# Optimization experiments

Hardware: AMD Instinct MI355X
Metric: run time of the kernel (lower is better)

Reference implementation:

```python
import jax, jax.numpy as jnp
import numpy as np

B, D = 32768, 256
M, K, V = 1024, 128, 128  # memory_units, key_size, memory_size


def setup_inputs() -> dict:
    key = jax.random.key(0)
    ks = jax.random.split(key, 13)
    g = lambda k, shape, fan: jax.random.normal(k, shape, jnp.float32) * (2.0 / sum(fan)) ** 0.5
    return {
        "x": jax.random.normal(ks[0], (B, D), jnp.float32),
        "Wk": g(ks[1], (D, K), (D, K)), "bk": jnp.zeros((K,), jnp.float32),
        "Wv": g(ks[2], (D, V), (D, V)), "bv": jnp.zeros((V,), jnp.float32),
        "Wq": g(ks[3], (D, K), (D, K)), "bq": jnp.zeros((K,), jnp.float32),
        "Wwr": g(ks[4], (M, M), (M, M)), "bwr": jnp.zeros((M,), jnp.float32),
        "Wrd": g(ks[5], (M, M), (M, M)), "brd": jnp.zeros((M,), jnp.float32),
        "key_memory": g(ks[6], (M, K), (M, K)),
        "value_memory": g(ks[7], (M, V), (M, V)),
    }


def reference(x, Wk, bk, Wv, bv, Wq, bq, Wwr, bwr, Wrd, brd, key_memory, value_memory):
    elu = jax.nn.elu
    key_vec = elu(x @ Wk + bk)      # [B, K]
    val_vec = elu(x @ Wv + bv)      # [B, V]
    qry_vec = elu(x @ Wq + bq)      # [B, K]

    # write attention: Dense(M, softmax) applied to [B, M] scores
    wscores = key_vec @ key_memory.T            # [B, M]
    write_w = jax.nn.softmax(wscores @ Wwr + bwr, axis=-1)  # [B, M]

    inv_b = jnp.float32(1.0 / B)
    # mean over batch of outer products == einsum / B (avoids [B, M, K] intermediate)
    key_mem_new = key_memory + jnp.einsum("bm,bk->mk", write_w, key_vec) * inv_b
    val_mem_new = value_memory + jnp.einsum("bm,bv->mv", write_w, val_vec) * inv_b

    # read uses the UPDATED memories (matches assign_add ordering in call)
    rscores = qry_vec @ key_mem_new.T            # [B, M]
    read_w = jax.nn.softmax(rscores @ Wrd + brd, axis=-1)
    read_vec = read_w @ val_mem_new              # [B, V]
    return read_vec
```

## Files before the change

### kernel.cpp

```cpp
#include <hip/hip_runtime.h>
#include <stdint.h>


typedef short bf16x8 __attribute__((ext_vector_type(8)));
typedef short s16x4  __attribute__((ext_vector_type(4)));
typedef float f32x4  __attribute__((ext_vector_type(4)));

#define MFMA(a, b, c) __builtin_amdgcn_mfma_f32_16x16x32_bf16((a), (b), (c), 0, 0, 0)

__device__ __forceinline__ short f2bf(float f) {
    union { float f; uint32_t u; } v; v.f = f;
    uint32_t r = (v.u + 0x7FFFu + ((v.u >> 16) & 1u)) >> 16;
    return (short)r;
}
__device__ __forceinline__ float bf2f(short h) {
    union { uint32_t u; float f; } v; v.u = ((uint32_t)(uint16_t)h) << 16;
    return v.f;
}
__device__ __forceinline__ uint32_t pack2(float a, float b) {
    return (uint32_t)(uint16_t)f2bf(a) | ((uint32_t)(uint16_t)f2bf(b) << 16);
}
__device__ __forceinline__ unsigned lds_addr(const void* p) {
    return (unsigned)(uintptr_t)(__attribute__((address_space(3))) const void*)p;
}
__device__ __forceinline__ s16x4 trrd(unsigned a) {
    s16x4 d;
    asm volatile("ds_read_b64_tr_b16 %0, %1" : "=v"(d) : "v"(a));
    return d;
}
__device__ __forceinline__ bf16x8 cat8(s16x4 lo, s16x4 hi) {
    bf16x8 r;
    r[0] = lo[0]; r[1] = lo[1]; r[2] = lo[2]; r[3] = lo[3];
    r[4] = hi[0]; r[5] = hi[1]; r[6] = hi[2]; r[7] = hi[3];
    return r;
}
#define GLDS(g, l) __builtin_amdgcn_global_load_lds(                          \
    (const __attribute__((address_space(1))) void*)(g),                       \
    (__attribute__((address_space(3))) void*)(l), 16, 0, 0)

__global__ void kw_kernel(const float* __restrict__ Wk, const float* __restrict__ Wv,
                          const float* __restrict__ Wq, short* __restrict__ wt) {
    const int c = blockIdx.x;
    const int d = threadIdx.x;
    const float* W = (c < 128) ? Wk : ((c < 256) ? Wv : Wq);
    wt[c * 256 + d] = f2bf(W[d * 128 + (c & 127)]);
}

__global__ __launch_bounds__(256) void proj_kernel(
    const float* __restrict__ x, const short* __restrict__ wt,
    const float* __restrict__ bk, const float* __restrict__ bv,
    const float* __restrict__ bq, short* __restrict__ kvq)
{
    const int tid = threadIdx.x;
    const int wave = tid >> 6, lane = tid & 63;
    const int l15 = lane & 15, lq = lane >> 4;
    const int r0 = blockIdx.x * 64;

    f32x4 acc[4][6];
    for (int i = 0; i < 4; ++i)
        for (int j = 0; j < 6; ++j) acc[i][j] = (f32x4){0.f, 0.f, 0.f, 0.f};

    for (int ks = 0; ks < 8; ++ks) {
        const int k0 = ks * 32 + lq * 8;
        bf16x8 a[4];
#pragma unroll
        for (int mf = 0; mf < 4; ++mf) {
            const float* xp = x + (long)(r0 + mf * 16 + l15) * 256 + k0;
            float4 u = *(const float4*)xp;
            float4 v = *(const float4*)(xp + 4);
            bf16x8 t;
            t[0] = f2bf(u.x); t[1] = f2bf(u.y); t[2] = f2bf(u.z); t[3] = f2bf(u.w);
            t[4] = f2bf(v.x); t[5] = f2bf(v.y); t[6] = f2bf(v.z); t[7] = f2bf(v.w);
            a[mf] = t;
        }
#pragma unroll
        for (int nf = 0; nf < 6; ++nf) {
            const int n = wave * 96 + nf * 16 + l15;
            bf16x8 b = *(const bf16x8*)(wt + n * 256 + k0);
#pragma unroll
            for (int mf = 0; mf < 4; ++mf) acc[mf][nf] = MFMA(a[mf], b, acc[mf][nf]);
        }
    }
#pragma unroll
    for (int nf = 0; nf < 6; ++nf) {
        const int col = wave * 96 + nf * 16 + l15;
        const float bias = (col < 128) ? bk[col] : ((col < 256) ? bv[col - 128] : bq[col - 256]);
#pragma unroll
        for (int mf = 0; mf < 4; ++mf) {
#pragma unroll
            for (int rr = 0; rr < 4; ++rr) {
                float v = acc[mf][nf][rr] + bias;
                v = (v > 0.f) ? v : (__expf(v) - 1.f);
                kvq[(long)(r0 + mf * 16 + lq * 4 + rr) * 384 + col] = f2bf(v);
            }
        }
    }
}

template <int COLS>
__global__ __launch_bounds__(256) void pgemm_kernel(
    const void* __restrict__ Agv, const void* __restrict__ Bgv,
    const int lda, const int ldb, const int rchunks, const int rstride,
    float* __restrict__ part)
{
    __shared__ __align__(16) short As[128][72];
    __shared__ __align__(16) short Bs[COLS][72];
    const int tid = threadIdx.x;
    const int wave = tid >> 6, lane = tid & 63;
    const int l15 = lane & 15, lq = lane >> 4;
    const int mt = blockIdx.x, rs = blockIdx.y;
    const long b0 = (long)rs * rstride;
    constexpr int NCF = COLS / 16;
    constexpr int CPT = COLS / 8;

    f32x4 acc[2][NCF];
    for (int s = 0; s < 2; ++s)
        for (int c = 0; c < NCF; ++c) acc[s][c] = (f32x4){0.f, 0.f, 0.f, 0.f};

    const int sr  = (tid & 31) * 2;
    const int am0 = (tid >> 5) * 16;
    const int bc0 = (tid >> 5) * CPT;

    for (int ch = 0; ch < rchunks; ++ch) {
        const long rb = b0 + (long)ch * 64;
        {
            const float* p0 = (const float*)Agv + (rb + sr) * lda + mt * 128 + am0;
            const float* p1 = p0 + lda;
#pragma unroll
            for (int j = 0; j < 16; ++j)
                *(uint32_t*)&As[am0 + j][sr] = pack2(p0[j], p1[j]);
        }
        {
            const float* p0 = (const float*)Bgv + (rb + sr) * ldb + bc0;
            const float* p1 = p0 + ldb;
#pragma unroll
            for (int j = 0; j < CPT; ++j)
                *(uint32_t*)&Bs[bc0 + j][sr] = pack2(p0[j], p1[j]);
        }
        __syncthreads();
#pragma unroll
        for (int ks = 0; ks < 2; ++ks) {
            bf16x8 a0 = *(const bf16x8*)&As[wave * 32 + l15][ks * 32 + lq * 8];
            bf16x8 a1 = *(const bf16x8*)&As[wave * 32 + 16 + l15][ks * 32 + lq * 8];
#pragma unroll
            for (int cf = 0; cf < NCF; ++cf) {
                bf16x8 b = *(const bf16x8*)&Bs[cf * 16 + l15][ks * 32 + lq * 8];
                acc[0][cf] = MFMA(a0, b, acc[0][cf]);
                acc[1][cf] = MFMA(a1, b, acc[1][cf]);
            }
        }
        __syncthreads();
    }
    float* pp = part + (long)rs * 1024 * COLS;
#pragma unroll
    for (int s = 0; s < 2; ++s)
#pragma unroll
        for (int cf = 0; cf < NCF; ++cf)
#pragma unroll
            for (int rr = 0; rr < 4; ++rr) {
                const int m = mt * 128 + wave * 32 + s * 16 + lq * 4 + rr;
                pp[(long)m * COLS + cf * 16 + l15] = acc[s][cf][rr];
            }
}

__global__ void finp_kernel(const float* __restrict__ part, short* __restrict__ pt) {
    const int i = blockIdx.x * 256 + threadIdx.x;
    float s = 0.f;
#pragma unroll
    for (int k = 0; k < 8; ++k) s += part[k * 131072 + i];
    pt[i] = f2bf(s);
}

__global__ __launch_bounds__(256) void eins_kernel(
    const short* __restrict__ w,
    const short* __restrict__ kvq,
    short* __restrict__ part)
{
    __shared__ __align__(16) short As[8192];
    __shared__ __align__(16) short Bs[8192];
    const int tid = threadIdx.x;
    const int wave = tid >> 6, lane = tid & 63;
    const int l15 = lane & 15, lq = lane >> 4;
    const int mt = blockIdx.x >> 1, ct = blockIdx.x & 1;
    const int ks = blockIdx.y;
    const long k0_blk = (long)ks * 1024;

    int aoff[4], boff[4];
    const short* ldsA[4];
    const short* ldsB[4];
#pragma unroll
    for (int q = 0; q < 4; ++q) {
        const int t = wave + q * 4;
        const int s = t * 8 + (lane >> 3);
        const int kl = (s & 15) * 4 + ((lane & 7) >> 1);
        const int m  = (s >> 4) * 16 + (lane & 1) * 8;
        aoff[q] = kl * 1024 + mt * 128 + m;
        boff[q] = kl * 384  + ct * 128 + m;
        ldsA[q] = &As[t * 512];
        ldsB[q] = &Bs[t * 512];
    }

    f32x4 acc[4][4];
    for (int i = 0; i < 4; ++i)
        for (int j = 0; j < 4; ++j) acc[i][j] = (f32x4){0.f, 0.f, 0.f, 0.f};

    const int wr = wave >> 1, wc = wave & 1;
    const unsigned trb  = lds_addr(As) + 2u * (l15 + lq * 64);
    const unsigned trbB = lds_addr(Bs) + 2u * (l15 + lq * 64);

    for (int ch = 0; ch < 16; ++ch) {
        const short* wa = w   + (k0_blk + ch * 64) * 1024;
        const short* kb = kvq + (k0_blk + ch * 64) * 384;
#pragma unroll
        for (int q = 0; q < 4; ++q) {
            GLDS(wa + aoff[q], ldsA[q]);
            GLDS(kb + boff[q], ldsB[q]);
        }
        __syncthreads();
#pragma unroll
        for (int kst = 0; kst < 2; ++kst) {
            s16x4 ah[4][2], bh[4][2];
#pragma unroll
            for (int f = 0; f < 4; ++f) {
#pragma unroll
                for (int h = 0; h < 2; ++h) {
                    ah[f][h] = trrd(trb  + 128u * ((wr * 4 + f) * 16 + kst * 8 + h * 4));
                    bh[f][h] = trrd(trbB + 128u * ((wc * 4 + f) * 16 + kst * 8 + h * 4));
                }
            }
            asm volatile("s_waitcnt lgkmcnt(0)" ::: "memory");
            __builtin_amdgcn_sched_barrier(0);
#pragma unroll
            for (int mf = 0; mf < 4; ++mf) {
                bf16x8 a = cat8(ah[mf][0], ah[mf][1]);
#pragma unroll
                for (int cf = 0; cf < 4; ++cf)
                    acc[mf][cf] = MFMA(a, cat8(bh[cf][0], bh[cf][1]), acc[mf][cf]);
            }
        }
        __syncthreads();
    }

    short* pp = part + ((long)ks * 1024 + mt * 128) * 256 + ct * 128;
#pragma unroll
    for (int mf = 0; mf < 4; ++mf)
#pragma unroll
        for (int cf = 0; cf < 4; ++cf)
#pragma unroll
            for (int rr = 0; rr < 4; ++rr) {
                const int m = wr * 64 + mf * 16 + lq * 4 + rr;
                const int c = wc * 64 + cf * 16 + l15;
                pp[(long)m * 256 + c] = f2bf(acc[mf][cf][rr]);
            }
}

__global__ void finmem_kernel(const short* __restrict__ part,
                              const float* __restrict__ km, const float* __restrict__ vm,
                              float* __restrict__ km_new, short* __restrict__ vmt) {
    const int m = blockIdx.x;
    const int c = threadIdx.x;
    float s = 0.f;
#pragma unroll
    for (int k = 0; k < 32; ++k) s += bf2f(part[k * 262144 + m * 256 + c]);
    s *= (1.0f / 32768.0f);
    if (c < 128) {
        km_new[m * 128 + c] = km[m * 128 + c] + s;
    } else {
        const int v = c - 128;
        vmt[v * 1024 + m] = f2bf(vm[m * 128 + v] + s);
    }
}

constexpr int LW = 1032;

template <int KOFF, int DOPV>
__global__ __launch_bounds__(256, 2) void smx_kernel(
    const short* __restrict__ kvq, const short* __restrict__ pt,
    const float* __restrict__ bias, const short* __restrict__ vmt,
    short* __restrict__ wout, float* __restrict__ out)
{
    __shared__ __align__(16) short L[32][LW];
    __shared__ float invs[32];
    const int tid = threadIdx.x;
    const int wave = tid >> 6, lane = tid & 63;
    const int l15 = lane & 15, lq = lane >> 4;
    const int r0 = blockIdx.x * 32;

    bf16x8 qf[2][4];
#pragma unroll
    for (int bg = 0; bg < 2; ++bg)
#pragma unroll
        for (int ks = 0; ks < 4; ++ks)
            qf[bg][ks] = *(const bf16x8*)(kvq + (long)(r0 + bg * 16 + l15) * 384 + KOFF + ks * 32 + lq * 8);

    for (int nt = 0; nt < 16; ++nt) {
        const int n0 = wave * 256 + nt * 16;
        f32x4 c0 = {0.f, 0.f, 0.f, 0.f}, c1 = {0.f, 0.f, 0.f, 0.f};
#pragma unroll
        for (int ks = 0; ks < 4; ++ks) {
            bf16x8 a = *(const bf16x8*)(pt + (n0 + l15) * 128 + ks * 32 + lq * 8);
            c0 = MFMA(a, qf[0][ks], c0);
            c1 = MFMA(a, qf[1][ks], c1);
        }
        *(uint2*)&L[l15][n0 + lq * 4]      = (uint2){pack2(c0[0], c0[1]), pack2(c0[2], c0[3])};
        *(uint2*)&L[16 + l15][n0 + lq * 4] = (uint2){pack2(c1[0], c1[1]), pack2(c1[2], c1[3])};
    }
    __syncthreads();

#pragma unroll
    for (int rep = 0; rep < 2; ++rep) {
        const int row = wave * 8 + rep * 4 + lq;
        float v[64], gm[8];
#pragma unroll
        for (int g = 0; g < 8; ++g) {
            bf16x8 t = *(const bf16x8*)&L[row][g * 128 + l15 * 8];
            float4 b0 = *(const float4*)(bias + g * 128 + l15 * 8);
            float4 b1 = *(const float4*)(bias + g * 128 + l15 * 8 + 4);
            v[g*8+0] = bf2f(t[0]) + b0.x; v[g*8+1] = bf2f(t[1]) + b0.y;
            v[g*8+2] = bf2f(t[2]) + b0.z; v[g*8+3] = bf2f(t[3]) + b0.w;
            v[g*8+4] = bf2f(t[4]) + b1.x; v[g*8+5] = bf2f(t[5]) + b1.y;
            v[g*8+6] = bf2f(t[6]) + b1.z; v[g*8+7] = bf2f(t[7]) + b1.w;
            gm[g] = fmaxf(fmaxf(fmaxf(v[g*8+0], v[g*8+1]), fmaxf(v[g*8+2], v[g*8+3])),
                          fmaxf(fmaxf(v[g*8+4], v[g*8+5]), fmaxf(v[g*8+6], v[g*8+7])));
        }
        float mx = fmaxf(fmaxf(fmaxf(gm[0], gm[1]), fmaxf(gm[2], gm[3])),
                         fmaxf(fmaxf(gm[4], gm[5]), fmaxf(gm[6], gm[7])));
#pragma unroll
        for (int off = 8; off; off >>= 1) mx = fmaxf(mx, __shfl_xor(mx, off));
        float gs[8];
#pragma unroll
        for (int g = 0; g < 8; ++g) {
            float s = 0.f;
#pragma unroll
            for (int j = 0; j < 8; ++j) { v[g*8+j] = __expf(v[g*8+j] - mx); s += v[g*8+j]; }
            gs[g] = s;
        }
        float sum = ((gs[0]+gs[1]) + (gs[2]+gs[3])) + ((gs[4]+gs[5]) + (gs[6]+gs[7]));
#pragma unroll
        for (int off = 8; off; off >>= 1) sum += __shfl_xor(sum, off);
        const float inv = 1.f / sum;

        if constexpr (!DOPV) {
#pragma unroll
            for (int g = 0; g < 8; ++g) {
                bf16x8 t;
#pragma unroll
                for (int j = 0; j < 8; ++j) t[j] = f2bf(v[g*8+j] * inv);
                *(bf16x8*)(wout + (long)(r0 + row) * 1024 + g * 128 + l15 * 8) = t;
            }
        } else {
#pragma unroll
            for (int g = 0; g < 8; ++g) {
                bf16x8 t;
#pragma unroll
                for (int j = 0; j < 8; ++j) t[j] = f2bf(v[g*8+j]);
                *(bf16x8*)&L[row][g * 128 + l15 * 8] = t;
            }
            if (l15 == 0) invs[row] = inv;
        }
    }

    if constexpr (DOPV) {
        __syncthreads();
        f32x4 acc[2][2];
        for (int i = 0; i < 2; ++i)
            for (int j = 0; j < 2; ++j) acc[i][j] = (f32x4){0.f, 0.f, 0.f, 0.f};
        for (int ks = 0; ks < 32; ++ks) {
            bf16x8 a0 = *(const bf16x8*)&L[l15][ks * 32 + lq * 8];
            bf16x8 a1 = *(const bf16x8*)&L[16 + l15][ks * 32 + lq * 8];
#pragma unroll
            for (int nf = 0; nf < 2; ++nf) {
                const int n = (wave * 2 + nf) * 16 + l15;
                bf16x8 b = *(const bf16x8*)(vmt + n * 1024 + ks * 32 + lq * 8);
                acc[0][nf] = MFMA(a0, b, acc[0][nf]);
                acc[1][nf] = MFMA(a1, b, acc[1][nf]);
            }
        }
#pragma unroll
        for (int mf = 0; mf < 2; ++mf)
#pragma unroll
            for (int nf = 0; nf < 2; ++nf)
#pragma unroll
                for (int rr = 0; rr < 4; ++rr) {
                    const int row = mf * 16 + lq * 4 + rr;
                    const int col = (wave * 2 + nf) * 16 + l15;
                    out[(long)(r0 + row) * 128 + col] = acc[mf][nf][rr] * invs[row];
                }
    }
}

extern "C" void kernel_launch(void* const* d_in, const int* in_sizes, int n_in,
                              void* d_out, int out_size, void* d_ws, size_t ws_size,
                              hipStream_t stream)
{
    const float* x   = (const float*)d_in[0];
    const float* Wk  = (const float*)d_in[1];
    const float* bk  = (const float*)d_in[2];
    const float* Wv  = (const float*)d_in[3];
    const float* bv  = (const float*)d_in[4];
    const float* Wq  = (const float*)d_in[5];
    const float* bq  = (const float*)d_in[6];
    const float* Wwr = (const float*)d_in[7];
    const float* bwr = (const float*)d_in[8];
    const float* Wrd = (const float*)d_in[9];
    const float* brd = (const float*)d_in[10];
    const float* km  = (const float*)d_in[11];
    const float* vm  = (const float*)d_in[12];
    float* out = (float*)d_out;

    char* ws = (char*)d_ws;
    short* kvq  = (short*)(ws + 0);
    short* w    = (short*)(ws + 25165824);
    float* part = (float*)(ws + 92274688);
    short* p1t  = (short*)(ws + 109051904);
    short* p2t  = (short*)(ws + 109314048);
    float* kmn  = (float*)(ws + 109576192);
    short* vmt  = (short*)(ws + 110100480);
    short* wt   = (short*)(ws + 110362624);
    if (ws_size < 110559232u) return;

    kw_kernel<<<384, 256, 0, stream>>>(Wk, Wv, Wq, wt);
    proj_kernel<<<512, 256, 0, stream>>>(x, wt, bk, bv, bq, kvq);
    pgemm_kernel<128><<<dim3(8, 8), 256, 0, stream>>>(Wwr, km, 1024, 128, 2, 128, part);
    finp_kernel<<<512, 256, 0, stream>>>(part, p1t);
    smx_kernel<0, 0><<<1024, 256, 0, stream>>>(kvq, p1t, bwr, nullptr, w, nullptr);
    eins_kernel<<<dim3(16, 32), 256, 0, stream>>>(w, kvq, (short*)part);
    finmem_kernel<<<1024, 256, 0, stream>>>((const short*)part, km, vm, kmn, vmt);
    pgemm_kernel<128><<<dim3(8, 8), 256, 0, stream>>>(Wrd, kmn, 1024, 128, 2, 128, part);
    finp_kernel<<<512, 256, 0, stream>>>(part, p2t);
    smx_kernel<256, 1><<<1024, 256, 0, stream>>>(kvq, p2t, brd, vmt, nullptr, out);
}
```

Measured before the change: 226.7 us.

## Keep softmax in registers and fold write normalization into key/value rows

Rewrites the two softmax kernels so score tiles stay in registers as packed bf16 instead of a 64KB LDS tile. Row max and row sum are combined across waves through small shared arrays. The write path stores unnormalized exponentials and instead scales the cached key/value projections by 1/sum in place, which moves the normalization into the einsum inputs. The read path feeds the register fragments straight into 16x16x16 MFMAs against the transposed value memory, then reduces across waves in LDS. This removes the large LDS footprint and its round-trips to raise occupancy, at the cost of an extra bf16 rounding on key/value and an in-place mutation of the workspace.

After: 275.0 us. 21.3% more time.

```diff
diff --git a/kernel.cpp b/kernel.cpp
--- a/kernel.cpp
+++ b/kernel.cpp
@@ -7,6 +7,11 @@
 typedef float f32x4  __attribute__((ext_vector_type(4)));
 
 #define MFMA(a, b, c) __builtin_amdgcn_mfma_f32_16x16x32_bf16((a), (b), (c), 0, 0, 0)
+
+__device__ __forceinline__ f32x4 MFMA16(s16x4 a, s16x4 b, f32x4 c) {
+    asm("v_mfma_f32_16x16x16_bf16 %0, %1, %2, %0" : "+v"(c) : "v"(a), "v"(b));
+    return c;
+}
 
 __device__ __forceinline__ short f2bf(float f) {
     union { float f; uint32_t u; } v; v.f = f;
@@ -19,6 +24,9 @@
 }
 __device__ __forceinline__ uint32_t pack2(float a, float b) {
     return (uint32_t)(uint16_t)f2bf(a) | ((uint32_t)(uint16_t)f2bf(b) << 16);
+}
+__device__ __forceinline__ s16x4 u2s(uint2 u) {
+    union { uint2 u; s16x4 s; } x; x.u = u; return x.s;
 }
 __device__ __forceinline__ unsigned lds_addr(const void* p) {
     return (unsigned)(uintptr_t)(__attribute__((address_space(3))) const void*)p;
@@ -271,121 +279,153 @@
     }
 }
 
-constexpr int LW = 1032;
-
 template <int KOFF, int DOPV>
-__global__ __launch_bounds__(256, 2) void smx_kernel(
-    const short* __restrict__ kvq, const short* __restrict__ pt,
+__global__ __launch_bounds__(256) void sfx_kernel(
+    const short* __restrict__ kvqc, const short* __restrict__ pt,
     const float* __restrict__ bias, const short* __restrict__ vmt,
-    short* __restrict__ wout, float* __restrict__ out)
+    short* __restrict__ eout, short* __restrict__ kvq_rw,
+    float* __restrict__ out)
 {
-    __shared__ __align__(16) short L[32][LW];
+    __shared__ float mred[4][32];
+    __shared__ float sred[4][32];
     __shared__ float invs[32];
+    __shared__ float red[DOPV ? 4 * 32 * 65 : 1];
+
     const int tid = threadIdx.x;
     const int wave = tid >> 6, lane = tid & 63;
     const int l15 = lane & 15, lq = lane >> 4;
     const int r0 = blockIdx.x * 32;
-
-    bf16x8 qf[2][4];
-#pragma unroll
-    for (int bg = 0; bg < 2; ++bg)
-#pragma unroll
-        for (int ks = 0; ks < 4; ++ks)
-            qf[bg][ks] = *(const bf16x8*)(kvq + (long)(r0 + bg * 16 + l15) * 384 + KOFF + ks * 32 + lq * 8);
-
+    const int n0 = wave * 256;
+
+    bf16x8 qf0[4], qf1[4];
+#pragma unroll
+    for (int ks = 0; ks < 4; ++ks) {
+        qf0[ks] = *(const bf16x8*)(kvqc + (long)(r0 + l15) * 384 + KOFF + ks * 32 + lq * 8);
+        qf1[ks] = *(const bf16x8*)(kvqc + (long)(r0 + 16 + l15) * 384 + KOFF + ks * 32 + lq * 8);
+    }
+
+    uint2 pk0[16], pk1[16];
+    float m0 = -3.0e38f, m1 = -3.0e38f;
     for (int nt = 0; nt < 16; ++nt) {
-        const int n0 = wave * 256 + nt * 16;
+        const short* prow = pt + (n0 + nt * 16 + l15) * 128 + lq * 8;
         f32x4 c0 = {0.f, 0.f, 0.f, 0.f}, c1 = {0.f, 0.f, 0.f, 0.f};
 #pragma unroll
         for (int ks = 0; ks < 4; ++ks) {
-            bf16x8 a = *(const bf16x8*)(pt + (n0 + l15) * 128 + ks * 32 + lq * 8);
-            c0 = MFMA(a, qf[0][ks], c0);
-            c1 = MFMA(a, qf[1][ks], c1);
-        }
-        *(uint2*)&L[l15][n0 + lq * 4]      = (uint2){pack2(c0[0], c0[1]), pack2(c0[2], c0[3])};
-        *(uint2*)&L[16 + l15][n0 + lq * 4] = (uint2){pack2(c1[0], c1[1]), pack2(c1[2], c1[3])};
-    }
+            bf16x8 a = *(const bf16x8*)(prow + ks * 32);
+            c0 = MFMA(a, qf0[ks], c0);
+            c1 = MFMA(a, qf1[ks], c1);
+        }
+        float4 b4 = *(const float4*)(bias + n0 + nt * 16 + lq * 4);
+        c0[0] += b4.x; c0[1] += b4.y; c0[2] += b4.z; c0[3] += b4.w;
+        c1[0] += b4.x; c1[1] += b4.y; c1[2] += b4.z; c1[3] += b4.w;
+        m0 = fmaxf(m0, fmaxf(fmaxf(c0[0], c0[1]), fmaxf(c0[2], c0[3])));
+        m1 = fmaxf(m1, fmaxf(fmaxf(c1[0], c1[1]), fmaxf(c1[2], c1[3])));
+        pk0[nt] = (uint2){pack2(c0[0], c0[1]), pack2(c0[2], c0[3])};
+        pk1[nt] = (uint2){pack2(c1[0], c1[1]), pack2(c1[2], c1[3])};
+    }
+
+    m0 = fmaxf(m0, __shfl_xor(m0, 16)); m0 = fmaxf(m0, __shfl_xor(m0, 32));
+    m1 = fmaxf(m1, __shfl_xor(m1, 16)); m1 = fmaxf(m1, __shfl_xor(m1, 32));
+    if (lane < 16) { mred[wave][lane] = m0; mred[wave][lane + 16] = m1; }
     __syncthreads();
-
-#pragma unroll
-    for (int rep = 0; rep < 2; ++rep) {
-        const int row = wave * 8 + rep * 4 + lq;
-        float v[64], gm[8];
-#pragma unroll
-        for (int g = 0; g < 8; ++g) {
-            bf16x8 t = *(const bf16x8*)&L[row][g * 128 + l15 * 8];
-            float4 b0 = *(const float4*)(bias + g * 128 + l15 * 8);
-            float4 b1 = *(const float4*)(bias + g * 128 + l15 * 8 + 4);
-            v[g*8+0] = bf2f(t[0]) + b0.x; v[g*8+1] = bf2f(t[1]) + b0.y;
-            v[g*8+2] = bf2f(t[2]) + b0.z; v[g*8+3] = bf2f(t[3]) + b0.w;
-            v[g*8+4] = bf2f(t[4]) + b1.x; v[g*8+5] = bf2f(t[5]) + b1.y;
-            v[g*8+6] = bf2f(t[6]) + b1.z; v[g*8+7] = bf2f(t[7]) + b1.w;
-            gm[g] = fmaxf(fmaxf(fmaxf(v[g*8+0], v[g*8+1]), fmaxf(v[g*8+2], v[g*8+3])),
-                          fmaxf(fmaxf(v[g*8+4], v[g*8+5]), fmaxf(v[g*8+6], v[g*8+7])));
-        }
-        float mx = fmaxf(fmaxf(fmaxf(gm[0], gm[1]), fmaxf(gm[2], gm[3])),
-                         fmaxf(fmaxf(gm[4], gm[5]), fmaxf(gm[6], gm[7])));
-#pragma unroll
-        for (int off = 8; off; off >>= 1) mx = fmaxf(mx, __shfl_xor(mx, off));
-        float gs[8];
-#pragma unroll
-        for (int g = 0; g < 8; ++g) {
-            float s = 0.f;
-#pragma unroll
-            for (int j = 0; j < 8; ++j) { v[g*8+j] = __expf(v[g*8+j] - mx); s += v[g*8+j]; }
-            gs[g] = s;
-        }
-        float sum = ((gs[0]+gs[1]) + (gs[2]+gs[3])) + ((gs[4]+gs[5]) + (gs[6]+gs[7]));
-#pragma unroll
-        for (int off = 8; off; off >>= 1) sum += __shfl_xor(sum, off);
-        const float inv = 1.f / sum;
-
-        if constexpr (!DOPV) {
-#pragma unroll
-            for (int g = 0; g < 8; ++g) {
-                bf16x8 t;
-#pragma unroll
-                for (int j = 0; j < 8; ++j) t[j] = f2bf(v[g*8+j] * inv);
-                *(bf16x8*)(wout + (long)(r0 + row) * 1024 + g * 128 + l15 * 8) = t;
-            }
-        } else {
-#pragma unroll
-            for (int g = 0; g < 8; ++g) {
-                bf16x8 t;
-#pragma unroll
-                for (int j = 0; j < 8; ++j) t[j] = f2bf(v[g*8+j]);
-                *(bf16x8*)&L[row][g * 128 + l15 * 8] = t;
-            }
-            if (l15 == 0) invs[row] = inv;
-        }
-    }
-
-    if constexpr (DOPV) {
+    float M0 = -3.0e38f, M1 = -3.0e38f;
+#pragma unroll
+    for (int wv = 0; wv < 4; ++wv) {
+        M0 = fmaxf(M0, mred[wv][l15]);
+        M1 = fmaxf(M1, mred[wv][16 + l15]);
+    }
+
+    float s0 = 0.f, s1 = 0.f;
+#pragma unroll
+    for (int nt = 0; nt < 16; ++nt) {
+        float e0 = __expf(bf2f((short)(pk0[nt].x & 0xffff)) - M0);
+        float e1 = __expf(bf2f((short)(pk0[nt].x >> 16)) - M0);
+        float e2 = __expf(bf2f((short)(pk0[nt].y & 0xffff)) - M0);
+        float e3 = __expf(bf2f((short)(pk0[nt].y >> 16)) - M0);
+        s0 += (e0 + e1) + (e2 + e3);
+        pk0[nt] = (uint2){pack2(e0, e1), pack2(e2, e3)};
+        float f0 = __expf(bf2f((short)(pk1[nt].x & 0xffff)) - M1);
+        float f1 = __expf(bf2f((short)(pk1[nt].x >> 16)) - M1);
+        float f2 = __expf(bf2f((short)(pk1[nt].y & 0xffff)) - M1);
+        float f3 = __expf(bf2f((short)(pk1[nt].y >> 16)) - M1);
+        s1 += (f0 + f1) + (f2 + f3);
+        pk1[nt] = (uint2){pack2(f0, f1), pack2(f2, f3)};
+    }
+    s0 += __shfl_xor(s0, 16); s0 += __shfl_xor(s0, 32);
+    s1 += __shfl_xor(s1, 16); s1 += __shfl_xor(s1, 32);
+    if (lane < 16) { sred[wave][lane] = s0; sred[wave][lane + 16] = s1; }
+    __syncthreads();
+    float S0 = 0.f, S1 = 0.f;
+#pragma unroll
+    for (int wv = 0; wv < 4; ++wv) {
+        S0 += sred[wv][l15];
+        S1 += sred[wv][16 + l15];
+    }
+    if (wave == 0 && lane < 16) {
+        invs[l15] = 1.f / S0;
+        invs[16 + l15] = 1.f / S1;
+    }
+
+    if constexpr (!DOPV) {
+        short* e0p = eout + (long)(r0 + l15) * 1024 + n0 + lq * 4;
+        short* e1p = eout + (long)(r0 + 16 + l15) * 1024 + n0 + lq * 4;
+#pragma unroll
+        for (int nt = 0; nt < 16; ++nt) {
+            *(uint2*)(e0p + nt * 16) = pk0[nt];
+            *(uint2*)(e1p + nt * 16) = pk1[nt];
+        }
         __syncthreads();
-        f32x4 acc[2][2];
-        for (int i = 0; i < 2; ++i)
-            for (int j = 0; j < 2; ++j) acc[i][j] = (f32x4){0.f, 0.f, 0.f, 0.f};
-        for (int ks = 0; ks < 32; ++ks) {
-            bf16x8 a0 = *(const bf16x8*)&L[l15][ks * 32 + lq * 8];
-            bf16x8 a1 = *(const bf16x8*)&L[16 + l15][ks * 32 + lq * 8];
-#pragma unroll
-            for (int nf = 0; nf < 2; ++nf) {
-                const int n = (wave * 2 + nf) * 16 + l15;
-                bf16x8 b = *(const bf16x8*)(vmt + n * 1024 + ks * 32 + lq * 8);
-                acc[0][nf] = MFMA(a0, b, acc[0][nf]);
-                acc[1][nf] = MFMA(a1, b, acc[1][nf]);
-            }
-        }
-#pragma unroll
-        for (int mf = 0; mf < 2; ++mf)
-#pragma unroll
-            for (int nf = 0; nf < 2; ++nf)
-#pragma unroll
-                for (int rr = 0; rr < 4; ++rr) {
-                    const int row = mf * 16 + lq * 4 + rr;
-                    const int col = (wave * 2 + nf) * 16 + l15;
-                    out[(long)(r0 + row) * 128 + col] = acc[mf][nf][rr] * invs[row];
+        const int row = tid >> 3;
+        const int col0 = (tid & 7) * 32;
+        const float sc = invs[row];
+        short* base = kvq_rw + (long)(r0 + row) * 384 + col0;
+#pragma unroll
+        for (int g = 0; g < 4; ++g) {
+            bf16x8 v = *(const bf16x8*)(base + g * 8);
+            bf16x8 t;
+#pragma unroll
+            for (int j = 0; j < 8; ++j) t[j] = f2bf(bf2f(v[j]) * sc);
+            *(bf16x8*)(base + g * 8) = t;
+        }
+    } else {
+#pragma unroll
+        for (int vp = 0; vp < 2; ++vp) {
+            f32x4 acc[2][4];
+#pragma unroll
+            for (int i = 0; i < 2; ++i)
+#pragma unroll
+                for (int j = 0; j < 4; ++j) acc[i][j] = (f32x4){0.f, 0.f, 0.f, 0.f};
+            for (int nt = 0; nt < 16; ++nt) {
+                s16x4 a0 = u2s(pk0[nt]);
+                s16x4 a1 = u2s(pk1[nt]);
+#pragma unroll
+                for (int vtl = 0; vtl < 4; ++vtl) {
+                    const int v = vp * 64 + vtl * 16 + l15;
+                    s16x4 b = *(const s16x4*)(vmt + v * 1024 + n0 + nt * 16 + lq * 4);
+                    acc[0][vtl] = MFMA16(a0, b, acc[0][vtl]);
+                    acc[1][vtl] = MFMA16(a1, b, acc[1][vtl]);
                 }
+            }
+#pragma unroll
+            for (int bs = 0; bs < 2; ++bs)
+#pragma unroll
+                for (int vtl = 0; vtl < 4; ++vtl)
+#pragma unroll
+                    for (int rr = 0; rr < 4; ++rr)
+                        red[wave * 2080 + (bs * 16 + lq * 4 + rr) * 65 + vtl * 16 + l15] =
+                            acc[bs][vtl][rr];
+            __syncthreads();
+            const int b = tid >> 3;
+            const int v0 = (tid & 7) * 8;
+            const float sc = invs[b];
+            float* op = out + (long)(r0 + b) * 128 + vp * 64 + v0;
+#pragma unroll
+            for (int j = 0; j < 8; ++j) {
+                const int idx = b * 65 + v0 + j;
+                op[j] = (red[idx] + red[2080 + idx] + red[4160 + idx] + red[6240 + idx]) * sc;
+            }
+            __syncthreads();
+        }
     }
 }
 
@@ -423,10 +463,10 @@
     proj_kernel<<<512, 256, 0, stream>>>(x, wt, bk, bv, bq, kvq);
     pgemm_kernel<128><<<dim3(8, 8), 256, 0, stream>>>(Wwr, km, 1024, 128, 2, 128, part);
     finp_kernel<<<512, 256, 0, stream>>>(part, p1t);
-    smx_kernel<0, 0><<<1024, 256, 0, stream>>>(kvq, p1t, bwr, nullptr, w, nullptr);
+    sfx_kernel<0, 0><<<1024, 256, 0, stream>>>(kvq, p1t, bwr, nullptr, w, kvq, nullptr);
     eins_kernel<<<dim3(16, 32), 256, 0, stream>>>(w, kvq, (short*)part);
     finmem_kernel<<<1024, 256, 0, stream>>>((const short*)part, km, vm, kmn, vmt);
     pgemm_kernel<128><<<dim3(8, 8), 256, 0, stream>>>(Wrd, kmn, 1024, 128, 2, 128, part);
     finp_kernel<<<512, 256, 0, stream>>>(part, p2t);
-    smx_kernel<256, 1><<<1024, 256, 0, stream>>>(kvq, p2t, brd, vmt, nullptr, out);
-}
+    sfx_kernel<256, 1><<<1024, 256, 0, stream>>>(kvq, p2t, brd, vmt, nullptr, nullptr, out);
+}
```

## Restructure softmax kernels into 64-row 1024-thread blocks with register-resident scores

Applied to the files above, without the earlier changes.

Replaces the templated smx_kernel with separate write (wexp) and read (rexp) kernels. Each uses 1024-thread blocks covering 64 rows. The query/key tile is staged once into swizzled LDS, and scores stay in fp32 MFMA accumulators instead of round-tripping through LDS as bf16. The softmax drops max-subtraction, exponentiating directly and reducing row sums across waves through shared memory. The read kernel then writes normalized weights to a large LDS buffer for the PV GEMM. This cuts LDS traffic and per-row reductions, but risks exp overflow for large scores and gives lower occupancy from the 132KB LDS footprint.

After: 203.9 us. 10.1% less time.

```diff
diff --git a/kernel.cpp b/kernel.cpp
--- a/kernel.cpp
+++ b/kernel.cpp
@@ -271,121 +271,207 @@
     }
 }
 
-constexpr int LW = 1032;
-
-template <int KOFF, int DOPV>
-__global__ __launch_bounds__(256, 2) void smx_kernel(
+__global__ __launch_bounds__(1024, 4) void wexp_kernel(
     const short* __restrict__ kvq, const short* __restrict__ pt,
-    const float* __restrict__ bias, const short* __restrict__ vmt,
-    short* __restrict__ wout, float* __restrict__ out)
+    const float* __restrict__ bias, short* __restrict__ wout)
 {
-    __shared__ __align__(16) short L[32][LW];
-    __shared__ float invs[32];
+    __shared__ __align__(16) char kt[16384];
+    __shared__ float sred[16][64];
+    __shared__ float invs[64];
     const int tid = threadIdx.x;
     const int wave = tid >> 6, lane = tid & 63;
     const int l15 = lane & 15, lq = lane >> 4;
-    const int r0 = blockIdx.x * 32;
-
-    bf16x8 qf[2][4];
-#pragma unroll
-    for (int bg = 0; bg < 2; ++bg)
-#pragma unroll
-        for (int ks = 0; ks < 4; ++ks)
-            qf[bg][ks] = *(const bf16x8*)(kvq + (long)(r0 + bg * 16 + l15) * 384 + KOFF + ks * 32 + lq * 8);
-
-    for (int nt = 0; nt < 16; ++nt) {
-        const int n0 = wave * 256 + nt * 16;
-        f32x4 c0 = {0.f, 0.f, 0.f, 0.f}, c1 = {0.f, 0.f, 0.f, 0.f};
-#pragma unroll
-        for (int ks = 0; ks < 4; ++ks) {
-            bf16x8 a = *(const bf16x8*)(pt + (n0 + l15) * 128 + ks * 32 + lq * 8);
-            c0 = MFMA(a, qf[0][ks], c0);
-            c1 = MFMA(a, qf[1][ks], c1);
-        }
-        *(uint2*)&L[l15][n0 + lq * 4]      = (uint2){pack2(c0[0], c0[1]), pack2(c0[2], c0[3])};
-        *(uint2*)&L[16 + l15][n0 + lq * 4] = (uint2){pack2(c1[0], c1[1]), pack2(c1[2], c1[3])};
-    }
-    __syncthreads();
-
-#pragma unroll
-    for (int rep = 0; rep < 2; ++rep) {
-        const int row = wave * 8 + rep * 4 + lq;
-        float v[64], gm[8];
-#pragma unroll
-        for (int g = 0; g < 8; ++g) {
-            bf16x8 t = *(const bf16x8*)&L[row][g * 128 + l15 * 8];
-            float4 b0 = *(const float4*)(bias + g * 128 + l15 * 8);
-            float4 b1 = *(const float4*)(bias + g * 128 + l15 * 8 + 4);
-            v[g*8+0] = bf2f(t[0]) + b0.x; v[g*8+1] = bf2f(t[1]) + b0.y;
-            v[g*8+2] = bf2f(t[2]) + b0.z; v[g*8+3] = bf2f(t[3]) + b0.w;
-            v[g*8+4] = bf2f(t[4]) + b1.x; v[g*8+5] = bf2f(t[5]) + b1.y;
-            v[g*8+6] = bf2f(t[6]) + b1.z; v[g*8+7] = bf2f(t[7]) + b1.w;
-            gm[g] = fmaxf(fmaxf(fmaxf(v[g*8+0], v[g*8+1]), fmaxf(v[g*8+2], v[g*8+3])),
-                          fmaxf(fmaxf(v[g*8+4], v[g*8+5]), fmaxf(v[g*8+6], v[g*8+7])));
-        }
-        float mx = fmaxf(fmaxf(fmaxf(gm[0], gm[1]), fmaxf(gm[2], gm[3])),
-                         fmaxf(fmaxf(gm[4], gm[5]), fmaxf(gm[6], gm[7])));
-#pragma unroll
-        for (int off = 8; off; off >>= 1) mx = fmaxf(mx, __shfl_xor(mx, off));
-        float gs[8];
-#pragma unroll
-        for (int g = 0; g < 8; ++g) {
-            float s = 0.f;
-#pragma unroll
-            for (int j = 0; j < 8; ++j) { v[g*8+j] = __expf(v[g*8+j] - mx); s += v[g*8+j]; }
-            gs[g] = s;
-        }
-        float sum = ((gs[0]+gs[1]) + (gs[2]+gs[3])) + ((gs[4]+gs[5]) + (gs[6]+gs[7]));
-#pragma unroll
-        for (int off = 8; off; off >>= 1) sum += __shfl_xor(sum, off);
-        const float inv = 1.f / sum;
-
-        if constexpr (!DOPV) {
-#pragma unroll
-            for (int g = 0; g < 8; ++g) {
-                bf16x8 t;
-#pragma unroll
-                for (int j = 0; j < 8; ++j) t[j] = f2bf(v[g*8+j] * inv);
-                *(bf16x8*)(wout + (long)(r0 + row) * 1024 + g * 128 + l15 * 8) = t;
-            }
-        } else {
-#pragma unroll
-            for (int g = 0; g < 8; ++g) {
-                bf16x8 t;
-#pragma unroll
-                for (int j = 0; j < 8; ++j) t[j] = f2bf(v[g*8+j]);
-                *(bf16x8*)&L[row][g * 128 + l15 * 8] = t;
-            }
-            if (l15 == 0) invs[row] = inv;
-        }
-    }
-
-    if constexpr (DOPV) {
-        __syncthreads();
-        f32x4 acc[2][2];
-        for (int i = 0; i < 2; ++i)
-            for (int j = 0; j < 2; ++j) acc[i][j] = (f32x4){0.f, 0.f, 0.f, 0.f};
-        for (int ks = 0; ks < 32; ++ks) {
-            bf16x8 a0 = *(const bf16x8*)&L[l15][ks * 32 + lq * 8];
-            bf16x8 a1 = *(const bf16x8*)&L[16 + l15][ks * 32 + lq * 8];
-#pragma unroll
-            for (int nf = 0; nf < 2; ++nf) {
-                const int n = (wave * 2 + nf) * 16 + l15;
-                bf16x8 b = *(const bf16x8*)(vmt + n * 1024 + ks * 32 + lq * 8);
-                acc[0][nf] = MFMA(a0, b, acc[0][nf]);
-                acc[1][nf] = MFMA(a1, b, acc[1][nf]);
-            }
-        }
-#pragma unroll
-        for (int mf = 0; mf < 2; ++mf)
-#pragma unroll
-            for (int nf = 0; nf < 2; ++nf)
-#pragma unroll
-                for (int rr = 0; rr < 4; ++rr) {
-                    const int row = mf * 16 + lq * 4 + rr;
-                    const int col = (wave * 2 + nf) * 16 + l15;
-                    out[(long)(r0 + row) * 128 + col] = acc[mf][nf][rr] * invs[row];
-                }
+    const int r0 = blockIdx.x * 64;
+    const int n0 = wave * 64;
+
+    {
+        const int row = tid >> 4;
+        const int colb = 16 * ((tid & 15) ^ (row & 7));
+        GLDS((const char*)kvq + (long)(r0 + row) * 768 + colb, kt + tid * 16);
+    }
+    __syncthreads();
+
+    f32x4 acc[4][4];
+#pragma unroll
+    for (int i = 0; i < 4; ++i)
+#pragma unroll
+        for (int j = 0; j < 4; ++j) acc[i][j] = (f32x4){0.f, 0.f, 0.f, 0.f};
+
+#pragma unroll
+    for (int ks = 0; ks < 4; ++ks) {
+        bf16x8 a[4], b[4];
+#pragma unroll
+        for (int nf = 0; nf < 4; ++nf)
+            a[nf] = *(const bf16x8*)(pt + (n0 + nf * 16 + l15) * 128 + ks * 32 + lq * 8);
+#pragma unroll
+        for (int bf = 0; bf < 4; ++bf) {
+            const int r = bf * 16 + l15;
+            const int cb = (ks * 64 + lq * 16) ^ ((r & 7) << 4);
+            b[bf] = *(const bf16x8*)(kt + r * 256 + cb);
+        }
+#pragma unroll
+        for (int nf = 0; nf < 4; ++nf)
+#pragma unroll
+            for (int bf = 0; bf < 4; ++bf)
+                acc[nf][bf] = MFMA(a[nf], b[bf], acc[nf][bf]);
+    }
+
+    float s[4] = {0.f, 0.f, 0.f, 0.f};
+#pragma unroll
+    for (int nf = 0; nf < 4; ++nf) {
+        float4 b4 = *(const float4*)(bias + n0 + nf * 16 + lq * 4);
+#pragma unroll
+        for (int bf = 0; bf < 4; ++bf) {
+            f32x4 t = acc[nf][bf];
+            t[0] = __expf(t[0] + b4.x);
+            t[1] = __expf(t[1] + b4.y);
+            t[2] = __expf(t[2] + b4.z);
+            t[3] = __expf(t[3] + b4.w);
+            acc[nf][bf] = t;
+            s[bf] += (t[0] + t[1]) + (t[2] + t[3]);
+        }
+    }
+#pragma unroll
+    for (int bf = 0; bf < 4; ++bf) {
+        s[bf] += __shfl_xor(s[bf], 16);
+        s[bf] += __shfl_xor(s[bf], 32);
+    }
+    if (lq == 0) {
+#pragma unroll
+        for (int bf = 0; bf < 4; ++bf) sred[wave][bf * 16 + l15] = s[bf];
+    }
+    __syncthreads();
+    if (tid < 64) {
+        float t = 0.f;
+#pragma unroll
+        for (int wv = 0; wv < 16; ++wv) t += sred[wv][tid];
+        invs[tid] = 1.f / t;
+    }
+    __syncthreads();
+
+#pragma unroll
+    for (int bf = 0; bf < 4; ++bf) {
+        const float iv = invs[bf * 16 + l15];
+        short* wp = wout + (long)(r0 + bf * 16 + l15) * 1024 + n0 + lq * 4;
+#pragma unroll
+        for (int nf = 0; nf < 4; ++nf) {
+            f32x4 t = acc[nf][bf];
+            *(uint2*)(wp + nf * 16) =
+                (uint2){pack2(t[0] * iv, t[1] * iv), pack2(t[2] * iv, t[3] * iv)};
+        }
+    }
+}
+
+__global__ __launch_bounds__(1024, 4) void rexp_kernel(
+    const short* __restrict__ kvq, const short* __restrict__ pt,
+    const float* __restrict__ bias, const short* __restrict__ vmt,
+    float* __restrict__ out)
+{
+    __shared__ __align__(16) char smem[132096];
+    __shared__ float sred[16][64];
+    __shared__ float invs[64];
+    short* Elds = (short*)smem;
+    char*  qt   = smem;
+    const int tid = threadIdx.x;
+    const int wave = tid >> 6, lane = tid & 63;
+    const int l15 = lane & 15, lq = lane >> 4;
+    const int r0 = blockIdx.x * 64;
+    const int n0 = wave * 64;
+
+    {
+        const int row = tid >> 4;
+        const int colb = 16 * ((tid & 15) ^ (row & 7));
+        GLDS((const char*)kvq + (long)(r0 + row) * 768 + 512 + colb, qt + tid * 16);
+    }
+    __syncthreads();
+
+    f32x4 acc[4][4];
+#pragma unroll
+    for (int i = 0; i < 4; ++i)
+#pragma unroll
+        for (int j = 0; j < 4; ++j) acc[i][j] = (f32x4){0.f, 0.f, 0.f, 0.f};
+
+#pragma unroll
+    for (int ks = 0; ks < 4; ++ks) {
+        bf16x8 a[4], b[4];
+#pragma unroll
+        for (int nf = 0; nf < 4; ++nf)
+            a[nf] = *(const bf16x8*)(pt + (n0 + nf * 16 + l15) * 128 + ks * 32 + lq * 8);
+#pragma unroll
+        for (int bf = 0; bf < 4; ++bf) {
+            const int r = bf * 16 + l15;
+            const int cb = (ks * 64 + lq * 16) ^ ((r & 7) << 4);
+            b[bf] = *(const bf16x8*)(qt + r * 256 + cb);
+        }
+#pragma unroll
+        for (int nf = 0; nf < 4; ++nf)
+#pragma unroll
+            for (int bf = 0; bf < 4; ++bf)
+                acc[nf][bf] = MFMA(a[nf], b[bf], acc[nf][bf]);
+    }
+
+    float s[4] = {0.f, 0.f, 0.f, 0.f};
+#pragma unroll
+    for (int nf = 0; nf < 4; ++nf) {
+        float4 b4 = *(const float4*)(bias + n0 + nf * 16 + lq * 4);
+#pragma unroll
+        for (int bf = 0; bf < 4; ++bf) {
+            f32x4 t = acc[nf][bf];
+            t[0] = __expf(t[0] + b4.x);
+            t[1] = __expf(t[1] + b4.y);
+            t[2] = __expf(t[2] + b4.z);
+            t[3] = __expf(t[3] + b4.w);
+            acc[nf][bf] = t;
+            s[bf] += (t[0] + t[1]) + (t[2] + t[3]);
+        }
+    }
+#pragma unroll
+    for (int bf = 0; bf < 4; ++bf) {
+        s[bf] += __shfl_xor(s[bf], 16);
+        s[bf] += __shfl_xor(s[bf], 32);
+    }
+    if (lq == 0) {
+#pragma unroll
+        for (int bf = 0; bf < 4; ++bf) sred[wave][bf * 16 + l15] = s[bf];
+    }
+    __syncthreads();
+    if (tid < 64) {
+        float t = 0.f;
+#pragma unroll
+        for (int wv = 0; wv < 16; ++wv) t += sred[wv][tid];
+        invs[tid] = 1.f / t;
+    }
+    __syncthreads();
+
+#pragma unroll
+    for (int bf = 0; bf < 4; ++bf) {
+        const float iv = invs[bf * 16 + l15];
+        short* ep = Elds + (bf * 16 + l15) * 1032 + n0 + lq * 4;
+#pragma unroll
+        for (int nf = 0; nf < 4; ++nf) {
+            f32x4 t = acc[nf][bf];
+            *(uint2*)(ep + nf * 16) =
+                (uint2){pack2(t[0] * iv, t[1] * iv), pack2(t[2] * iv, t[3] * iv)};
+        }
+    }
+    __syncthreads();
+
+    const int vf = wave >> 1;
+    const int bfp = (wave & 1) * 2;
+    f32x4 pv0 = {0.f, 0.f, 0.f, 0.f}, pv1 = {0.f, 0.f, 0.f, 0.f};
+    const short* er0 = Elds + (bfp * 16 + l15) * 1032 + lq * 8;
+    const short* er1 = er0 + 16 * 1032;
+    const short* vp  = vmt + (vf * 16 + l15) * 1024 + lq * 8;
+#pragma unroll 8
+    for (int ks = 0; ks < 32; ++ks) {
+        bf16x8 bv = *(const bf16x8*)(vp + ks * 32);
+        pv0 = MFMA(*(const bf16x8*)(er0 + ks * 32), bv, pv0);
+        pv1 = MFMA(*(const bf16x8*)(er1 + ks * 32), bv, pv1);
+    }
+#pragma unroll
+    for (int rr = 0; rr < 4; ++rr) {
+        out[(long)(r0 + bfp * 16 + lq * 4 + rr) * 128 + vf * 16 + l15] = pv0[rr];
+        out[(long)(r0 + (bfp + 1) * 16 + lq * 4 + rr) * 128 + vf * 16 + l15] = pv1[rr];
     }
 }
 
@@ -423,10 +509,10 @@
     proj_kernel<<<512, 256, 0, stream>>>(x, wt, bk, bv, bq, kvq);
     pgemm_kernel<128><<<dim3(8, 8), 256, 0, stream>>>(Wwr, km, 1024, 128, 2, 128, part);
     finp_kernel<<<512, 256, 0, stream>>>(part, p1t);
-    smx_kernel<0, 0><<<1024, 256, 0, stream>>>(kvq, p1t, bwr, nullptr, w, nullptr);
+    wexp_kernel<<<512, 1024, 0, stream>>>(kvq, p1t, bwr, w);
     eins_kernel<<<dim3(16, 32), 256, 0, stream>>>(w, kvq, (short*)part);
     finmem_kernel<<<1024, 256, 0, stream>>>((const short*)part, km, vm, kmn, vmt);
     pgemm_kernel<128><<<dim3(8, 8), 256, 0, stream>>>(Wrd, kmn, 1024, 128, 2, 128, part);
     finp_kernel<<<512, 256, 0, stream>>>(part, p2t);
-    smx_kernel<256, 1><<<1024, 256, 0, stream>>>(kvq, p2t, brd, vmt, nullptr, out);
-}
+    rexp_kernel<<<512, 1024, 0, stream>>>(kvq, p2t, brd, vmt, out);
+}
```
